# Performance work log

Measured on AMD Instinct MI355X. Metric: run time of the kernel, lower is better.

Reference implementation:

```python
import jax, jax.numpy as jnp
import numpy as np

SR = 10  # self.sr in the torch module

def _linear_params(key, fan_in, fan_out):
    kw, kb = jax.random.split(key)
    bound = 1.0 / np.sqrt(fan_in)
    W = jax.random.uniform(kw, (fan_out, fan_in), jnp.float32, -bound, bound)
    b = jax.random.uniform(kb, (fan_out,), jnp.float32, -bound, bound)
    return W, b

def setup_inputs() -> dict:
    key = jax.random.key(0)
    ks = jax.random.split(key, 6)
    P, H = 2048, 1024
    R = C = P * SR
    X = jax.random.normal(ks[0], (R, C), jnp.float32)
    p = jax.random.randint(ks[1], (P,), 0, 64, jnp.int32)
    W1, b1 = _linear_params(ks[2], 1, H)
    W2, b2 = _linear_params(ks[3], H, H)
    W3, b3 = _linear_params(ks[4], H, H)
    W4, b4 = _linear_params(ks[5], H, 1)
    return {"X": X, "p": p, "W1": W1, "b1": b1, "W2": W2, "b2": b2,
            "W3": W3, "b3": b3, "W4": W4, "b4": b4}

def _forward(X, p, W1, b1, W2, b2, W3, b3, W4, b4):
    P = p.shape[0]
    C = X.shape[1]
    # shift_rows: only rows i*SR for i in [0, P-2] are populated; all other
    # rows of the shifted matrix are NaN and contribute 0 sum / 0 count below.
    rows = X[jnp.arange(P - 1) * SR]                      # (P-1, C)
    shifts = p[: P - 1]
    # torch.roll(x, s): out[j] = x[(j - s) mod C]
    cols = (jnp.arange(C)[None, :] - shifts[:, None]) % C  # (P-1, C)
    shifted = jnp.take_along_axis(rows, cols, axis=1)      # (P-1, C)
    # nan_mean over rows (NaN rows of the full matrix drop out identically)
    mask = jnp.isnan(shifted)
    col_sum = jnp.where(mask, 0.0, shifted).sum(axis=0)
    col_cnt = (~mask).sum(axis=0).astype(jnp.float32)
    m = jnp.where(col_cnt > 0, col_sum / col_cnt, jnp.float32(jnp.nan))  # (C,)
    # fill_nan_with_last_value: serial forward-fill (index 0 kept as-is)
    def step(last, xi):
        v = jnp.where(jnp.isnan(xi), last, xi)
        return v, v
    _, rest = jax.lax.scan(step, m[0], m[1:])
    filled = jnp.concatenate([m[:1], rest])                # (C,)
    x = filled[::SR][:P][:, None]                          # (P, 1)
    h = jax.nn.relu(x @ W1.T + b1)
    h = jax.nn.relu(h @ W2.T + b2)
    h = jax.nn.relu(h @ W3.T + b3)
    y = h @ W4.T + b4                                      # (P, 1)
    return y[:, 0]

def reference(X, p, W1, b1, W2, b2, W3, b3, W4, b4):
    return _forward(X, p, W1, b1, W2, b2, W3, b3, W4, b4)
```

## Files before the change

kernel.cpp:

```cpp
#include <hip/hip_runtime.h>
#include <hip/hip_bf16.h>

#define CC 20480
#define PP 2048
#define NROWS 2047
#define SRR 10
#define HH 1024
#define NCH 64

typedef __attribute__((ext_vector_type(8))) short short8;
typedef __attribute__((ext_vector_type(4))) float f32x4;

__device__ __forceinline__ void split_bf16(float v, unsigned short& hi, unsigned short& lo) {
    __hip_bfloat16 h = __float2bfloat16(v);
    float r = v - __bfloat162float(h);
    __hip_bfloat16 l2 = __float2bfloat16(r);
    hi = *(unsigned short*)&h;
    lo = *(unsigned short*)&l2;
}

__global__ __launch_bounds__(256) void pre_k(const float* __restrict__ X,
                                             const int* __restrict__ p,
                                             float* __restrict__ psum,
                                             const float* __restrict__ W2,
                                             unsigned short* __restrict__ w2h,
                                             unsigned short* __restrict__ w2l,
                                             const float* __restrict__ W3,
                                             unsigned short* __restrict__ w3h,
                                             unsigned short* __restrict__ w3l) {
    int b = blockIdx.x, t = threadIdx.x;
    if (b < 512) {
        int k = (b & 7) * 256 + t;
        int chunk = b >> 3;
        int r0 = chunk * 32;
        int r1 = r0 + 32; if (r1 > NROWS) r1 = NROWS;
        float s = 0.f;
        int base = SRR * k;
        for (int i = r0; i < r1; ++i) {
            int col = base - p[i]; if (col < 0) col += CC;
            s += X[(size_t)i * (size_t)(SRR * CC) + col];
        }
        psum[chunk * PP + k] = s;
        return;
    }
    int bb = b - 512;
    const float* src; unsigned short *dh, *dl;
    if (bb < 256) { src = W2; dh = w2h; dl = w2l; }
    else { src = W3; dh = w3h; dl = w3l; bb -= 256; }
    int idx = bb * 4096 + t * 16;
    #pragma unroll
    for (int q = 0; q < 4; ++q) {
        float4 v = *(const float4*)&src[idx + q * 4];
        float vv[4] = {v.x, v.y, v.z, v.w};
        ushort hi4[4], lo4[4];
        #pragma unroll
        for (int i = 0; i < 4; ++i) split_bf16(vv[i], hi4[i], lo4[i]);
        *(ushort4*)&dh[idx + q * 4] = *(ushort4*)hi4;
        *(ushort4*)&dl[idx + q * 4] = *(ushort4*)lo4;
    }
}

__global__ __launch_bounds__(256) void prep2_k(const float* __restrict__ psum,
                                               const float* __restrict__ W1,
                                               const float* __restrict__ b1,
                                               unsigned short* __restrict__ h1h,
                                               unsigned short* __restrict__ h1l) {
    __shared__ float xv[8];
    int b = blockIdx.x, t = threadIdx.x;
    int kl = t >> 5;
    int c = t & 31;
    int k = b * 8 + kl;
    float s = psum[c * PP + k] + psum[(c + 32) * PP + k];
    #pragma unroll
    for (int m2 = 1; m2 < 32; m2 <<= 1) s += __shfl_xor(s, m2, 64);
    if (c == 0) xv[kl] = s * (1.0f / (float)NROWS);
    __syncthreads();
    int o0 = (t & 63) * 16;
    float w[16], bb2[16];
    #pragma unroll
    for (int q = 0; q < 4; ++q) {
        float4 wv = *(const float4*)&W1[o0 + q * 4];
        float4 bv = *(const float4*)&b1[o0 + q * 4];
        w[q*4+0] = wv.x; w[q*4+1] = wv.y; w[q*4+2] = wv.z; w[q*4+3] = wv.w;
        bb2[q*4+0] = bv.x; bb2[q*4+1] = bv.y; bb2[q*4+2] = bv.z; bb2[q*4+3] = bv.w;
    }
    #pragma unroll
    for (int pass = 0; pass < 2; ++pass) {
        int r = (t >> 6) + 4 * pass;
        float x = xv[r];
        ushort hi16[16], lo16[16];
        #pragma unroll
        for (int i = 0; i < 16; ++i) {
            float v = x * w[i] + bb2[i];
            v = v > 0.f ? v : 0.f;
            split_bf16(v, hi16[i], lo16[i]);
        }
        size_t base = (size_t)(b * 8 + r) * HH + o0;
        *(short8*)&h1h[base] = *(short8*)hi16;
        *(short8*)&h1h[base + 8] = *(short8*)&hi16[8];
        *(short8*)&h1l[base] = *(short8*)lo16;
        *(short8*)&h1l[base + 8] = *(short8*)&lo16[8];
    }
}

__device__ __forceinline__ void gload16(const unsigned short* g, unsigned short* lds) {
    __builtin_amdgcn_global_load_lds(
        (const __attribute__((address_space(1))) void*)g,
        (__attribute__((address_space(3))) void*)lds,
        16, 0, 0);
}

#define BM 128
#define BN 64
#define BK 32
#define NBY 16
#define BUFE 12288

template<int OUT>
__global__ __launch_bounds__(512, 2) void gemm3x_k(
    const unsigned short* __restrict__ Ah, const unsigned short* __restrict__ Al,
    const unsigned short* __restrict__ Bh, const unsigned short* __restrict__ Bl,
    const float* __restrict__ bias,
    unsigned short* __restrict__ Ch, unsigned short* __restrict__ Cl,
    const float* __restrict__ W4, float* __restrict__ partial,
    int M, int N, int K)
{
    __shared__ unsigned short lds[2][BUFE];
    int lin = blockIdx.x;
    int v = (lin & 7) * (gridDim.x >> 3) + (lin >> 3);
    int bx = v >> 4, by = v & (NBY - 1);
    int bm = bx * BM, bn = by * BN;
    int t = threadIdx.x, w = t >> 6, l = t & 63;
    int lr = l & 15, lk = l >> 4;
    int wr = w >> 1, wc = w & 1;

    size_t offA = (size_t)(bm + w * 16 + lr) * K + lk * 8;
    size_t offB = (size_t)(bn + (w & 3) * 16 + lr) * K + lk * 8;

#define STAGE(buf, k0)                                                   \
    do {                                                                 \
        unsigned short* L = lds[buf];                                    \
        gload16(Ah + offA + (k0), L + w * 512);                          \
        gload16(Al + offA + (k0), L + 4096 + w * 512);                   \
        if (w < 4) gload16(Bh + offB + (k0), L + 8192 + w * 512);        \
        else       gload16(Bl + offB + (k0), L + 10240 + (w - 4) * 512); \
    } while (0)

    f32x4 acc[2][2];
    #pragma unroll
    for (int i = 0; i < 2; ++i)
        #pragma unroll
        for (int j = 0; j < 2; ++j) acc[i][j] = (f32x4)(0.f);

    STAGE(0, 0);

    int nt = K / BK;
    for (int tt = 0; tt < nt; ++tt) {
        int cur = tt & 1;
        if (tt + 1 < nt) {
            STAGE(cur ^ 1, (tt + 1) * BK);
            asm volatile("s_waitcnt vmcnt(3)" ::: "memory");
        } else {
            asm volatile("s_waitcnt vmcnt(0)" ::: "memory");
        }
        __builtin_amdgcn_s_barrier();
        __builtin_amdgcn_sched_barrier(0);
        unsigned short* L = lds[cur];
        short8 ah2[2], al2[2], bh2[2], bl2[2];
        #pragma unroll
        for (int mi = 0; mi < 2; ++mi) {
            ah2[mi] = *(const short8*)&L[(wr * 2 + mi) * 512 + l * 8];
            al2[mi] = *(const short8*)&L[4096 + (wr * 2 + mi) * 512 + l * 8];
        }
        #pragma unroll
        for (int ni = 0; ni < 2; ++ni) {
            bh2[ni] = *(const short8*)&L[8192 + (wc * 2 + ni) * 512 + l * 8];
            bl2[ni] = *(const short8*)&L[10240 + (wc * 2 + ni) * 512 + l * 8];
        }
        asm volatile("s_waitcnt lgkmcnt(0)" ::: "memory");
        __builtin_amdgcn_sched_barrier(0);
        __builtin_amdgcn_s_setprio(1);
        #pragma unroll
        for (int mi = 0; mi < 2; ++mi)
            #pragma unroll
            for (int ni = 0; ni < 2; ++ni) {
                acc[mi][ni] = __builtin_amdgcn_mfma_f32_16x16x32_bf16(ah2[mi], bh2[ni], acc[mi][ni], 0, 0, 0);
                acc[mi][ni] = __builtin_amdgcn_mfma_f32_16x16x32_bf16(ah2[mi], bl2[ni], acc[mi][ni], 0, 0, 0);
                acc[mi][ni] = __builtin_amdgcn_mfma_f32_16x16x32_bf16(al2[mi], bh2[ni], acc[mi][ni], 0, 0, 0);
            }
        __builtin_amdgcn_s_setprio(0);
        __builtin_amdgcn_s_barrier();
        __builtin_amdgcn_sched_barrier(0);
    }
#undef STAGE

    float bv[2];
    #pragma unroll
    for (int ni = 0; ni < 2; ++ni) bv[ni] = bias[bn + wc * 32 + ni * 16 + lr];
    if (OUT == 1) {
        #pragma unroll
        for (int mi = 0; mi < 2; ++mi)
            #pragma unroll
            for (int ni = 0; ni < 2; ++ni)
                #pragma unroll
                for (int r = 0; r < 4; ++r) {
                    int row = bm + wr * 32 + mi * 16 + lk * 4 + r;
                    int col = bn + wc * 32 + ni * 16 + lr;
                    float vv = acc[mi][ni][r] + bv[ni];
                    vv = vv > 0.f ? vv : 0.f;
                    unsigned short hi, lo;
                    split_bf16(vv, hi, lo);
                    Ch[(size_t)row * N + col] = hi;
                    Cl[(size_t)row * N + col] = lo;
                }
    } else {
        float w4v[2];
        #pragma unroll
        for (int ni = 0; ni < 2; ++ni) w4v[ni] = W4[bn + wc * 32 + ni * 16 + lr];
        #pragma unroll
        for (int mi = 0; mi < 2; ++mi) {
            float ps[4];
            #pragma unroll
            for (int r = 0; r < 4; ++r) {
                float acc_d = 0.f;
                #pragma unroll
                for (int ni = 0; ni < 2; ++ni) {
                    float vv = acc[mi][ni][r] + bv[ni];
                    vv = vv > 0.f ? vv : 0.f;
                    acc_d += vv * w4v[ni];
                }
                ps[r] = acc_d;
            }
            #pragma unroll
            for (int r = 0; r < 4; ++r) {
                #pragma unroll
                for (int m2 = 1; m2 < 16; m2 <<= 1) ps[r] += __shfl_xor(ps[r], m2, 64);
            }
            if (lr == 0) {
                #pragma unroll
                for (int r = 0; r < 4; ++r) {
                    int row = bm + wr * 32 + mi * 16 + lk * 4 + r;
                    partial[(size_t)row * 32 + by * 2 + wc] = ps[r];
                }
            }
        }
    }
}

__global__ __launch_bounds__(256) void ysum_k(const float* __restrict__ partial,
                                              const float* __restrict__ b4,
                                              float* __restrict__ y) {
    int r = blockIdx.x * 256 + threadIdx.x;
    float s = 0.f;
    #pragma unroll
    for (int q = 0; q < 8; ++q) {
        float4 v = *(const float4*)&partial[(size_t)r * 32 + q * 4];
        s += v.x + v.y + v.z + v.w;
    }
    y[r] = s + b4[0];
}

extern "C" void kernel_launch(void* const* d_in, const int* in_sizes, int n_in,
                              void* d_out, int out_size, void* d_ws, size_t ws_size,
                              hipStream_t stream) {
    const float* X  = (const float*)d_in[0];
    const int*   p  = (const int*)d_in[1];
    const float* W1 = (const float*)d_in[2];
    const float* b1 = (const float*)d_in[3];
    const float* W2 = (const float*)d_in[4];
    const float* b2 = (const float*)d_in[5];
    const float* W3 = (const float*)d_in[6];
    const float* b3 = (const float*)d_in[7];
    const float* W4 = (const float*)d_in[8];
    const float* b4 = (const float*)d_in[9];
    float* out = (float*)d_out;

    char* ws = (char*)d_ws;
    size_t off = 0;
    float* psum = (float*)(ws + off); off += (size_t)NCH * PP * 4;
    unsigned short* h1h = (unsigned short*)(ws + off); off += (size_t)PP * HH * 2;
    unsigned short* h1l = (unsigned short*)(ws + off); off += (size_t)PP * HH * 2;
    unsigned short* h2h = (unsigned short*)(ws + off); off += (size_t)PP * HH * 2;
    unsigned short* h2l = (unsigned short*)(ws + off); off += (size_t)PP * HH * 2;
    unsigned short* w2h = (unsigned short*)(ws + off); off += (size_t)HH * HH * 2;
    unsigned short* w2l = (unsigned short*)(ws + off); off += (size_t)HH * HH * 2;
    unsigned short* w3h = (unsigned short*)(ws + off); off += (size_t)HH * HH * 2;
    unsigned short* w3l = (unsigned short*)(ws + off); off += (size_t)HH * HH * 2;
    float* partial = (float*)(ws + off); off += (size_t)PP * 32 * 4;

    pre_k<<<1024, 256, 0, stream>>>(X, p, psum, W2, w2h, w2l, W3, w3h, w3l);
    prep2_k<<<256, 256, 0, stream>>>(psum, W1, b1, h1h, h1l);
    gemm3x_k<1><<<(PP / BM) * (HH / BN), 512, 0, stream>>>(
        h1h, h1l, w2h, w2l, b2, h2h, h2l, (const float*)nullptr, (float*)nullptr, PP, HH, HH);
    gemm3x_k<2><<<(PP / BM) * (HH / BN), 512, 0, stream>>>(
        h2h, h2l, w3h, w3l, b3, (unsigned short*)nullptr, (unsigned short*)nullptr, W4, partial, PP, HH, HH);
    ysum_k<<<PP / 256, 256, 0, stream>>>(partial, b4, out);
}
```

Baseline: 88.95 us.

## Fuse first layer (h1 computation and bf16 split) into the first GEMM's A operand

Removes the prep2 kernel and the h1 hi/lo buffers. The first GEMM now computes relu(x*W1+b1) on the fly in registers from the per-row means and LDS-cached W1/b1, and streams only the W2 tiles through LDS. This cuts one launch and roughly 8 MB of global write plus read traffic, at the cost of extra VALU work per K-step inside the GEMM loop. It also drops the explicit lgkmcnt wait and moves setprio earlier in the second GEMM.

New measurement: 83.97 us. 1.06x faster.

```diff
diff --git a/kernel.cpp b/kernel.cpp
--- a/kernel.cpp
+++ b/kernel.cpp
@@ -60,49 +60,6 @@
     }
 }
 
-__global__ __launch_bounds__(256) void prep2_k(const float* __restrict__ psum,
-                                               const float* __restrict__ W1,
-                                               const float* __restrict__ b1,
-                                               unsigned short* __restrict__ h1h,
-                                               unsigned short* __restrict__ h1l) {
-    __shared__ float xv[8];
-    int b = blockIdx.x, t = threadIdx.x;
-    int kl = t >> 5;
-    int c = t & 31;
-    int k = b * 8 + kl;
-    float s = psum[c * PP + k] + psum[(c + 32) * PP + k];
-    #pragma unroll
-    for (int m2 = 1; m2 < 32; m2 <<= 1) s += __shfl_xor(s, m2, 64);
-    if (c == 0) xv[kl] = s * (1.0f / (float)NROWS);
-    __syncthreads();
-    int o0 = (t & 63) * 16;
-    float w[16], bb2[16];
-    #pragma unroll
-    for (int q = 0; q < 4; ++q) {
-        float4 wv = *(const float4*)&W1[o0 + q * 4];
-        float4 bv = *(const float4*)&b1[o0 + q * 4];
-        w[q*4+0] = wv.x; w[q*4+1] = wv.y; w[q*4+2] = wv.z; w[q*4+3] = wv.w;
-        bb2[q*4+0] = bv.x; bb2[q*4+1] = bv.y; bb2[q*4+2] = bv.z; bb2[q*4+3] = bv.w;
-    }
-    #pragma unroll
-    for (int pass = 0; pass < 2; ++pass) {
-        int r = (t >> 6) + 4 * pass;
-        float x = xv[r];
-        ushort hi16[16], lo16[16];
-        #pragma unroll
-        for (int i = 0; i < 16; ++i) {
-            float v = x * w[i] + bb2[i];
-            v = v > 0.f ? v : 0.f;
-            split_bf16(v, hi16[i], lo16[i]);
-        }
-        size_t base = (size_t)(b * 8 + r) * HH + o0;
-        *(short8*)&h1h[base] = *(short8*)hi16;
-        *(short8*)&h1h[base + 8] = *(short8*)&hi16[8];
-        *(short8*)&h1l[base] = *(short8*)lo16;
-        *(short8*)&h1l[base + 8] = *(short8*)&lo16[8];
-    }
-}
-
 __device__ __forceinline__ void gload16(const unsigned short* g, unsigned short* lds) {
     __builtin_amdgcn_global_load_lds(
         (const __attribute__((address_space(1))) void*)g,
@@ -113,29 +70,145 @@
 #define BM 128
 #define BN 64
 #define BK 32
-#define NBY 16
-#define BUFE 12288
-
-template<int OUT>
-__global__ __launch_bounds__(512, 2) void gemm3x_k(
-    const unsigned short* __restrict__ Ah, const unsigned short* __restrict__ Al,
+
+__global__ __launch_bounds__(512, 2) void gemm1_k(
+    const float* __restrict__ psum,
+    const float* __restrict__ W1, const float* __restrict__ b1,
     const unsigned short* __restrict__ Bh, const unsigned short* __restrict__ Bl,
-    const float* __restrict__ bias,
-    unsigned short* __restrict__ Ch, unsigned short* __restrict__ Cl,
-    const float* __restrict__ W4, float* __restrict__ partial,
-    int M, int N, int K)
+    const float* __restrict__ b2,
+    unsigned short* __restrict__ Ch, unsigned short* __restrict__ Cl)
 {
-    __shared__ unsigned short lds[2][BUFE];
+    __shared__ unsigned short Bb[2][4096];
+    __shared__ float w1f[1024], b1f[1024], xv[128];
+
     int lin = blockIdx.x;
-    int v = (lin & 7) * (gridDim.x >> 3) + (lin >> 3);
-    int bx = v >> 4, by = v & (NBY - 1);
+    int v = (lin & 7) * 32 + (lin >> 3);
+    int bx = v >> 4, by = v & 15;
     int bm = bx * BM, bn = by * BN;
     int t = threadIdx.x, w = t >> 6, l = t & 63;
     int lr = l & 15, lk = l >> 4;
     int wr = w >> 1, wc = w & 1;
 
-    size_t offA = (size_t)(bm + w * 16 + lr) * K + lk * 8;
-    size_t offB = (size_t)(bn + (w & 3) * 16 + lr) * K + lk * 8;
+    size_t offB = (size_t)(bn + (w & 3) * 16 + lr) * HH + lk * 8;
+#define BSTAGE(buf, k0)                                                      \
+    do {                                                                     \
+        if (w < 4) gload16(Bh + offB + (k0), Bb[buf] + w * 512);             \
+        else       gload16(Bl + offB + (k0), Bb[buf] + 2048 + (w - 4) * 512);\
+    } while (0)
+
+    BSTAGE(0, 0);
+    {
+        int row = t >> 2, q = t & 3;
+        float s = 0.f;
+        #pragma unroll
+        for (int j = 0; j < 16; ++j) s += psum[(q * 16 + j) * PP + bm + row];
+        s += __shfl_xor(s, 1, 64);
+        s += __shfl_xor(s, 2, 64);
+        if (q == 0) xv[row] = s * (1.0f / (float)NROWS);
+        if (t < 256) *(float4*)&w1f[t * 4] = *(const float4*)&W1[t * 4];
+        else *(float4*)&b1f[(t - 256) * 4] = *(const float4*)&b1[(t - 256) * 4];
+    }
+    __syncthreads();
+
+    float x0 = xv[wr * 32 + lr], x1 = xv[wr * 32 + 16 + lr];
+
+    f32x4 acc[2][2];
+    #pragma unroll
+    for (int i = 0; i < 2; ++i)
+        #pragma unroll
+        for (int j = 0; j < 2; ++j) acc[i][j] = (f32x4)(0.f);
+
+    int nt = HH / BK;
+    for (int tt = 0; tt < nt; ++tt) {
+        int cur = tt & 1;
+        if (tt + 1 < nt) {
+            BSTAGE(cur ^ 1, (tt + 1) * BK);
+            asm volatile("s_waitcnt vmcnt(1)" ::: "memory");
+        } else {
+            asm volatile("s_waitcnt vmcnt(0)" ::: "memory");
+        }
+        __builtin_amdgcn_s_barrier();
+        __builtin_amdgcn_sched_barrier(0);
+        __builtin_amdgcn_s_setprio(1);
+        int k0 = tt * BK;
+        float4 wva = *(const float4*)&w1f[k0 + lk * 8];
+        float4 wvb = *(const float4*)&w1f[k0 + lk * 8 + 4];
+        float4 bva = *(const float4*)&b1f[k0 + lk * 8];
+        float4 bvb = *(const float4*)&b1f[k0 + lk * 8 + 4];
+        float wv[8] = {wva.x, wva.y, wva.z, wva.w, wvb.x, wvb.y, wvb.z, wvb.w};
+        float bv2[8] = {bva.x, bva.y, bva.z, bva.w, bvb.x, bvb.y, bvb.z, bvb.w};
+        ushort ahh[2][8], all2[2][8];
+        #pragma unroll
+        for (int mi = 0; mi < 2; ++mi) {
+            float xm = mi ? x1 : x0;
+            #pragma unroll
+            for (int j = 0; j < 8; ++j) {
+                float h = fmaf(xm, wv[j], bv2[j]);
+                h = h > 0.f ? h : 0.f;
+                split_bf16(h, ahh[mi][j], all2[mi][j]);
+            }
+        }
+        short8 bh2[2], bl2[2];
+        #pragma unroll
+        for (int ni = 0; ni < 2; ++ni) {
+            bh2[ni] = *(const short8*)&Bb[cur][(wc * 2 + ni) * 512 + l * 8];
+            bl2[ni] = *(const short8*)&Bb[cur][2048 + (wc * 2 + ni) * 512 + l * 8];
+        }
+        #pragma unroll
+        for (int mi = 0; mi < 2; ++mi) {
+            short8 ah2 = *(short8*)ahh[mi];
+            short8 al2 = *(short8*)all2[mi];
+            #pragma unroll
+            for (int ni = 0; ni < 2; ++ni) {
+                acc[mi][ni] = __builtin_amdgcn_mfma_f32_16x16x32_bf16(ah2, bh2[ni], acc[mi][ni], 0, 0, 0);
+                acc[mi][ni] = __builtin_amdgcn_mfma_f32_16x16x32_bf16(ah2, bl2[ni], acc[mi][ni], 0, 0, 0);
+                acc[mi][ni] = __builtin_amdgcn_mfma_f32_16x16x32_bf16(al2, bh2[ni], acc[mi][ni], 0, 0, 0);
+            }
+        }
+        __builtin_amdgcn_s_setprio(0);
+        __builtin_amdgcn_sched_barrier(0);
+        __builtin_amdgcn_s_barrier();
+        __builtin_amdgcn_sched_barrier(0);
+    }
+#undef BSTAGE
+
+    float bv[2];
+    #pragma unroll
+    for (int ni = 0; ni < 2; ++ni) bv[ni] = b2[bn + wc * 32 + ni * 16 + lr];
+    #pragma unroll
+    for (int mi = 0; mi < 2; ++mi)
+        #pragma unroll
+        for (int ni = 0; ni < 2; ++ni)
+            #pragma unroll
+            for (int r = 0; r < 4; ++r) {
+                int row = bm + wr * 32 + mi * 16 + lk * 4 + r;
+                int col = bn + wc * 32 + ni * 16 + lr;
+                float vv = acc[mi][ni][r] + bv[ni];
+                vv = vv > 0.f ? vv : 0.f;
+                unsigned short hi, lo;
+                split_bf16(vv, hi, lo);
+                Ch[(size_t)row * HH + col] = hi;
+                Cl[(size_t)row * HH + col] = lo;
+            }
+}
+
+__global__ __launch_bounds__(512, 2) void gemm2_k(
+    const unsigned short* __restrict__ Ah, const unsigned short* __restrict__ Al,
+    const unsigned short* __restrict__ Bh, const unsigned short* __restrict__ Bl,
+    const float* __restrict__ b3,
+    const float* __restrict__ W4, float* __restrict__ partial)
+{
+    __shared__ unsigned short lds[2][12288];
+    int lin = blockIdx.x;
+    int v = (lin & 7) * 32 + (lin >> 3);
+    int bx = v >> 4, by = v & 15;
+    int bm = bx * BM, bn = by * BN;
+    int t = threadIdx.x, w = t >> 6, l = t & 63;
+    int lr = l & 15, lk = l >> 4;
+    int wr = w >> 1, wc = w & 1;
+
+    size_t offA = (size_t)(bm + w * 16 + lr) * HH + lk * 8;
+    size_t offB = (size_t)(bn + (w & 3) * 16 + lr) * HH + lk * 8;
 
 #define STAGE(buf, k0)                                                   \
     do {                                                                 \
@@ -154,7 +227,7 @@
 
     STAGE(0, 0);
 
-    int nt = K / BK;
+    int nt = HH / BK;
     for (int tt = 0; tt < nt; ++tt) {
         int cur = tt & 1;
         if (tt + 1 < nt) {
@@ -165,6 +238,7 @@
         }
         __builtin_amdgcn_s_barrier();
         __builtin_amdgcn_sched_barrier(0);
+        __builtin_amdgcn_s_setprio(1);
         unsigned short* L = lds[cur];
         short8 ah2[2], al2[2], bh2[2], bl2[2];
         #pragma unroll
@@ -177,9 +251,6 @@
             bh2[ni] = *(const short8*)&L[8192 + (wc * 2 + ni) * 512 + l * 8];
             bl2[ni] = *(const short8*)&L[10240 + (wc * 2 + ni) * 512 + l * 8];
         }
-        asm volatile("s_waitcnt lgkmcnt(0)" ::: "memory");
-        __builtin_amdgcn_sched_barrier(0);
-        __builtin_amdgcn_s_setprio(1);
         #pragma unroll
         for (int mi = 0; mi < 2; ++mi)
             #pragma unroll
@@ -189,59 +260,42 @@
                 acc[mi][ni] = __builtin_amdgcn_mfma_f32_16x16x32_bf16(al2[mi], bh2[ni], acc[mi][ni], 0, 0, 0);
             }
         __builtin_amdgcn_s_setprio(0);
+        __builtin_amdgcn_sched_barrier(0);
         __builtin_amdgcn_s_barrier();
         __builtin_amdgcn_sched_barrier(0);
     }
 #undef STAGE
 
-    float bv[2];
-    #pragma unroll
-    for (int ni = 0; ni < 2; ++ni) bv[ni] = bias[bn + wc * 32 + ni * 16 + lr];
-    if (OUT == 1) {
-        #pragma unroll
-        for (int mi = 0; mi < 2; ++mi)
-            #pragma unroll
-            for (int ni = 0; ni < 2; ++ni)
-                #pragma unroll
-                for (int r = 0; r < 4; ++r) {
-                    int row = bm + wr * 32 + mi * 16 + lk * 4 + r;
-                    int col = bn + wc * 32 + ni * 16 + lr;
-                    float vv = acc[mi][ni][r] + bv[ni];
-                    vv = vv > 0.f ? vv : 0.f;
-                    unsigned short hi, lo;
-                    split_bf16(vv, hi, lo);
-                    Ch[(size_t)row * N + col] = hi;
-                    Cl[(size_t)row * N + col] = lo;
-                }
-    } else {
-        float w4v[2];
-        #pragma unroll
-        for (int ni = 0; ni < 2; ++ni) w4v[ni] = W4[bn + wc * 32 + ni * 16 + lr];
-        #pragma unroll
-        for (int mi = 0; mi < 2; ++mi) {
-            float ps[4];
+    float bv[2], w4v[2];
+    #pragma unroll
+    for (int ni = 0; ni < 2; ++ni) {
+        bv[ni]  = b3[bn + wc * 32 + ni * 16 + lr];
+        w4v[ni] = W4[bn + wc * 32 + ni * 16 + lr];
+    }
+    #pragma unroll
+    for (int mi = 0; mi < 2; ++mi) {
+        float ps[4];
+        #pragma unroll
+        for (int r = 0; r < 4; ++r) {
+            float acc_d = 0.f;
+            #pragma unroll
+            for (int ni = 0; ni < 2; ++ni) {
+                float vv = acc[mi][ni][r] + bv[ni];
+                vv = vv > 0.f ? vv : 0.f;
+                acc_d += vv * w4v[ni];
+            }
+            ps[r] = acc_d;
+        }
+        #pragma unroll
+        for (int r = 0; r < 4; ++r) {
+            #pragma unroll
+            for (int m2 = 1; m2 < 16; m2 <<= 1) ps[r] += __shfl_xor(ps[r], m2, 64);
+        }
+        if (lr == 0) {
             #pragma unroll
             for (int r = 0; r < 4; ++r) {
-                float acc_d = 0.f;
-                #pragma unroll
-                for (int ni = 0; ni < 2; ++ni) {
-                    float vv = acc[mi][ni][r] + bv[ni];
-                    vv = vv > 0.f ? vv : 0.f;
-                    acc_d += vv * w4v[ni];
-                }
-                ps[r] = acc_d;
-            }
-            #pragma unroll
-            for (int r = 0; r < 4; ++r) {
-                #pragma unroll
-                for (int m2 = 1; m2 < 16; m2 <<= 1) ps[r] += __shfl_xor(ps[r], m2, 64);
-            }
-            if (lr == 0) {
-                #pragma unroll
-                for (int r = 0; r < 4; ++r) {
-                    int row = bm + wr * 32 + mi * 16 + lk * 4 + r;
-                    partial[(size_t)row * 32 + by * 2 + wc] = ps[r];
-                }
+                int row = bm + wr * 32 + mi * 16 + lk * 4 + r;
+                partial[(size_t)row * 32 + by * 2 + wc] = ps[r];
             }
         }
     }
@@ -278,8 +332,6 @@
     char* ws = (char*)d_ws;
     size_t off = 0;
     float* psum = (float*)(ws + off); off += (size_t)NCH * PP * 4;
-    unsigned short* h1h = (unsigned short*)(ws + off); off += (size_t)PP * HH * 2;
-    unsigned short* h1l = (unsigned short*)(ws + off); off += (size_t)PP * HH * 2;
     unsigned short* h2h = (unsigned short*)(ws + off); off += (size_t)PP * HH * 2;
     unsigned short* h2l = (unsigned short*)(ws + off); off += (size_t)PP * HH * 2;
     unsigned short* w2h = (unsigned short*)(ws + off); off += (size_t)HH * HH * 2;
@@ -289,10 +341,7 @@
     float* partial = (float*)(ws + off); off += (size_t)PP * 32 * 4;
 
     pre_k<<<1024, 256, 0, stream>>>(X, p, psum, W2, w2h, w2l, W3, w3h, w3l);
-    prep2_k<<<256, 256, 0, stream>>>(psum, W1, b1, h1h, h1l);
-    gemm3x_k<1><<<(PP / BM) * (HH / BN), 512, 0, stream>>>(
-        h1h, h1l, w2h, w2l, b2, h2h, h2l, (const float*)nullptr, (float*)nullptr, PP, HH, HH);
-    gemm3x_k<2><<<(PP / BM) * (HH / BN), 512, 0, stream>>>(
-        h2h, h2l, w3h, w3l, b3, (unsigned short*)nullptr, (unsigned short*)nullptr, W4, partial, PP, HH, HH);
+    gemm1_k<<<256, 512, 0, stream>>>(psum, W1, b1, w2h, w2l, b2, h2h, h2l);
+    gemm2_k<<<256, 512, 0, stream>>>(h2h, h2l, w3h, w3l, b3, W4, partial);
     ysum_k<<<PP / 256, 256, 0, stream>>>(partial, b4, out);
 }
```
